# Optimization experiments

Measured on AMD Instinct MI355X. Metric: run time of the kernel, lower is better.

## Reference

```python
import jax, jax.numpy as jnp
import numpy as np

N_NODES = 100000
F_DIM = 128      # graph.num_node_features
TE_DIM = 32      # te_emb_dim
D = F_DIM + TE_DIM  # attention embed_dim = 160
B = 4096         # number of target nodes (batched python loop)
K = 64           # candidates per target
TAU = 1.0
THRESHOLD = 0.2
EPS = 1e-10


def setup_inputs() -> dict:
    key = jax.random.key(0)
    ks = jax.random.split(key, 16)
    inp = {
        "x": jax.random.normal(ks[0], (N_NODES, F_DIM), dtype=jnp.float32),
        "target_node_ids": jax.random.randint(ks[1], (B,), 0, N_NODES),
        "target_node_times": jax.random.randint(ks[2], (B,), 1, 10000),
        "neighbor_ids": jax.random.randint(ks[3], (B, K), 0, N_NODES),
        "edge_time": jax.random.randint(ks[4], (B, K), 0, 10000),
        "edge_weight": jax.random.uniform(ks[5], (B, K), dtype=jnp.float32),
        "gumbel_u": jax.random.uniform(ks[6], (B, K), dtype=jnp.float32),
        # TemporalEncoding params: te(t) = cos(t * w + b)
        "te_w": jax.random.normal(ks[7], (TE_DIM,), dtype=jnp.float32),
        "te_b": jax.random.normal(ks[8], (TE_DIM,), dtype=jnp.float32),
        # MultiheadAttention params (packed qkv like torch)
        "in_proj_w": jax.random.normal(ks[9], (3 * D, D), dtype=jnp.float32) / np.sqrt(D),
        "in_proj_b": jnp.zeros((3 * D,), dtype=jnp.float32),
        "out_w": jax.random.normal(ks[10], (D, D), dtype=jnp.float32) / np.sqrt(D),
        "out_b": jnp.zeros((D,), dtype=jnp.float32),
        # MLP: Linear(D+1 -> 1) + LeakyReLU
        "mlp_w": jax.random.normal(ks[11], (D + 1,), dtype=jnp.float32) / np.sqrt(D + 1),
        "mlp_b": jnp.zeros((1,), dtype=jnp.float32),
    }
    return inp


def reference(x, target_node_ids, target_node_times, neighbor_ids, edge_time,
              edge_weight, gumbel_u, te_w, te_b, in_proj_w, in_proj_b,
              out_w, out_b, mlp_w, mlp_b):
    # --- build target embedding: [B, D]
    t_x = x[target_node_ids]                                          # [B, F]
    t_te = jnp.cos(target_node_times[:, None].astype(jnp.float32) * te_w + te_b)  # [B, TE]
    q_in = jnp.concatenate([t_x, t_te], axis=-1)                      # [B, D]

    # --- candidate embeddings: [B, K, D]
    c_x = x[neighbor_ids]                                             # [B, K, F]
    c_te = jnp.cos(edge_time[..., None].astype(jnp.float32) * te_w + te_b)        # [B, K, TE]
    kv_in = jnp.concatenate([c_x, c_te], axis=-1)                     # [B, K, D]

    # --- single-head MultiheadAttention (eval mode, 1 query per target)
    Wq, Wk, Wv = in_proj_w[:D], in_proj_w[D:2 * D], in_proj_w[2 * D:]
    bq, bk, bv = in_proj_b[:D], in_proj_b[D:2 * D], in_proj_b[2 * D:]
    q = q_in @ Wq.T + bq                                              # [B, D]
    k = jnp.einsum('bkf,df->bkd', kv_in, Wk) + bk                     # [B, K, D]
    v = jnp.einsum('bkf,df->bkd', kv_in, Wv) + bv                     # [B, K, D]
    scores = jnp.einsum('bd,bkd->bk', q, k) / jnp.sqrt(jnp.float32(D))
    attn_w = jax.nn.softmax(scores, axis=-1)                          # [B, K]
    ctx = jnp.einsum('bk,bkd->bd', attn_w, v)                         # [B, D]
    attn_output = ctx @ out_w.T + out_b                               # [B, D]

    # --- gumbel-softmax mask over attention weights (soft, then threshold)
    g = -jnp.log(-jnp.log(gumbel_u + EPS) + EPS)                      # gumbel(0,1)
    y_soft = jax.nn.softmax((attn_w + g) / TAU, axis=-1)
    candidate_mask = y_soft > THRESHOLD                               # [B, K] bool

    # --- MLP edge-weight update: Linear(D+1 -> 1) + LeakyReLU
    mlp_in = jnp.concatenate(
        [jnp.broadcast_to(attn_output[:, None, :], (attn_output.shape[0], edge_weight.shape[1], attn_output.shape[1])),
         edge_weight[..., None]], axis=-1)                            # [B, K, D+1]
    new_edge_weight = jax.nn.leaky_relu(jnp.einsum('bkf,f->bk', mlp_in, mlp_w) + mlp_b[0])  # [B, K]

    return attn_output, new_edge_weight, candidate_mask
```

## Files before the change

### kernel.cpp

```cpp
#include <hip/hip_runtime.h>

#define F_DIM 128
#define TE_DIM 32
#define DD 160
#define NB 4096
#define KK 64
#define ROWS 4
#define LD 164
#define XH_STRIDE 168
#define KT 16

#define WS_M   0
#define WS_V2  25600
#define WS_C   51200
#define WS_U   51360
#define WS_B2  51520
#define WS_S0  51680
#define WS_TE  51684
#define TAB_T  10000
#define TAB_N  (TAB_T * TE_DIM)
#define TAB_BLOCKS 250
#define SETUP_BASE (2 * DD + 3)

__device__ __forceinline__ float dot4acc(const float4 w, const float4 v, float a) {
    a = fmaf(w.x, v.x, a);
    a = fmaf(w.y, v.y, a);
    a = fmaf(w.z, v.z, a);
    a = fmaf(w.w, v.w, a);
    return a;
}

__device__ __forceinline__ float wave_max(float v) {
    #pragma unroll
    for (int off = 32; off > 0; off >>= 1) v = fmaxf(v, __shfl_xor(v, off, 64));
    return v;
}
__device__ __forceinline__ float wave_sum(float v) {
    #pragma unroll
    for (int off = 32; off > 0; off >>= 1) v += __shfl_xor(v, off, 64);
    return v;
}

__device__ __forceinline__ void gemv_rows(
    const float* __restrict__ W, const float* __restrict__ bias,
    const float (*vin)[LD], float (*vout)[LD], int tid)
{
    const int r  = tid & 3;
    const int dl = tid >> 2;
    const float4* v4 = (const float4*)vin[r];
    const float4* w0 = (const float4*)(W + (long)dl * DD);
    const float4* w1 = (const float4*)(W + (long)(dl + 64) * DD);
    float a0 = bias[dl];
    float a1 = bias[dl + 64];
    if (dl < 32) {
        const float4* w2 = (const float4*)(W + (long)(dl + 128) * DD);
        float a2 = bias[dl + 128];
        #pragma unroll 8
        for (int f = 0; f < 40; ++f) {
            const float4 v = v4[f];
            a0 = dot4acc(w0[f], v, a0);
            a1 = dot4acc(w1[f], v, a1);
            a2 = dot4acc(w2[f], v, a2);
        }
        vout[r][dl]       = a0;
        vout[r][dl + 64]  = a1;
        vout[r][dl + 128] = a2;
    } else {
        #pragma unroll 8
        for (int f = 0; f < 40; ++f) {
            const float4 v = v4[f];
            a0 = dot4acc(w0[f], v, a0);
            a1 = dot4acc(w1[f], v, a1);
        }
        vout[r][dl]      = a0;
        vout[r][dl + 64] = a1;
    }
}

__global__ __launch_bounds__(256)
void setup_kernel(const float* __restrict__ ipw, const float* __restrict__ ipb,
                  const float* __restrict__ ow,  const float* __restrict__ ob,
                  const float* __restrict__ te_w, const float* __restrict__ te_b,
                  float* __restrict__ ws)
{
    const int blk = blockIdx.x;
    const int t   = threadIdx.x;
    const float inv = 0.07905694150420949f;

    __shared__ float s_vec[DD];

    if (blk >= SETUP_BASE) {
        const int g0 = (blk - SETUP_BASE) * 256 + t;
        #pragma unroll
        for (int it = 0; it < 5; ++it) {
            const int g = g0 + it * (TAB_BLOCKS * 256);
            const int tt = g >> 5, d = g & 31;
            ws[WS_TE + g] = cosf(fmaf((float)tt, te_w[d], te_b[d]));
        }
        return;
    }

    if (blk < DD) {
        const float* wk = ipw + DD * DD;
        if (t < DD) s_vec[t] = wk[(long)t * DD + blk];
        __syncthreads();
        if (t < DD) {
            float a0 = 0.f, a1 = 0.f, a2 = 0.f, a3 = 0.f;
            #pragma unroll 4
            for (int d = 0; d < DD; d += 4) {
                a0 = fmaf(s_vec[d],     ipw[(long)d * DD + t],       a0);
                a1 = fmaf(s_vec[d + 1], ipw[(long)(d + 1) * DD + t], a1);
                a2 = fmaf(s_vec[d + 2], ipw[(long)(d + 2) * DD + t], a2);
                a3 = fmaf(s_vec[d + 3], ipw[(long)(d + 3) * DD + t], a3);
            }
            ws[WS_M + blk * DD + t] = (a0 + a1 + a2 + a3) * inv;
        }
    } else if (blk < 2 * DD) {
        const int i = blk - DD;
        const float* wv = ipw + 2 * DD * DD;
        if (t < DD) s_vec[t] = ow[(long)i * DD + t];
        __syncthreads();
        if (t < DD) {
            float a0 = 0.f, a1 = 0.f, a2 = 0.f, a3 = 0.f;
            #pragma unroll 4
            for (int d = 0; d < DD; d += 4) {
                a0 = fmaf(s_vec[d],     wv[(long)d * DD + t],       a0);
                a1 = fmaf(s_vec[d + 1], wv[(long)(d + 1) * DD + t], a1);
                a2 = fmaf(s_vec[d + 2], wv[(long)(d + 2) * DD + t], a2);
                a3 = fmaf(s_vec[d + 3], wv[(long)(d + 3) * DD + t], a3);
            }
            ws[WS_V2 + i * DD + t] = a0 + a1 + a2 + a3;
        }
    } else if (blk == 2 * DD) {
        const float* wk = ipw + DD * DD;
        if (t < DD) s_vec[t] = ipb[t];
        __syncthreads();
        if (t < DD) {
            float a0 = 0.f, a1 = 0.f, a2 = 0.f, a3 = 0.f;
            #pragma unroll 4
            for (int d = 0; d < DD; d += 4) {
                a0 = fmaf(s_vec[d],     wk[(long)d * DD + t],       a0);
                a1 = fmaf(s_vec[d + 1], wk[(long)(d + 1) * DD + t], a1);
                a2 = fmaf(s_vec[d + 2], wk[(long)(d + 2) * DD + t], a2);
                a3 = fmaf(s_vec[d + 3], wk[(long)(d + 3) * DD + t], a3);
            }
            ws[WS_C + t] = (a0 + a1 + a2 + a3) * inv;
        }
    } else if (blk == 2 * DD + 1) {
        if (t < DD) s_vec[t] = ipb[DD + t];
        __syncthreads();
        if (t < DD) {
            float a0 = 0.f, a1 = 0.f, a2 = 0.f, a3 = 0.f;
            #pragma unroll 4
            for (int d = 0; d < DD; d += 4) {
                a0 = fmaf(s_vec[d],     ipw[(long)d * DD + t],       a0);
                a1 = fmaf(s_vec[d + 1], ipw[(long)(d + 1) * DD + t], a1);
                a2 = fmaf(s_vec[d + 2], ipw[(long)(d + 2) * DD + t], a2);
                a3 = fmaf(s_vec[d + 3], ipw[(long)(d + 3) * DD + t], a3);
            }
            ws[WS_U + t] = (a0 + a1 + a2 + a3) * inv;
        }
    } else {
        if (t < DD) s_vec[t] = ipb[2 * DD + t];
        __syncthreads();
        if (t < DD) {
            const float* owr = ow + (long)t * DD;
            float a0 = 0.f, a1 = 0.f, a2 = 0.f, a3 = 0.f;
            #pragma unroll 4
            for (int d = 0; d < DD; d += 4) {
                a0 = fmaf(s_vec[d],     owr[d],     a0);
                a1 = fmaf(s_vec[d + 1], owr[d + 1], a1);
                a2 = fmaf(s_vec[d + 2], owr[d + 2], a2);
                a3 = fmaf(s_vec[d + 3], owr[d + 3], a3);
            }
            ws[WS_B2 + t] = ob[t] + (a0 + a1 + a2 + a3);
        }
        if (t >= 192) {
            const int lane = t - 192;
            float p = ipb[lane] * ipb[DD + lane];
            p = fmaf(ipb[lane + 64], ipb[DD + lane + 64], p);
            if (lane < 32) p = fmaf(ipb[lane + 128], ipb[DD + lane + 128], p);
            const float s = wave_sum(p);
            if (lane == 0) ws[WS_S0] = s * inv;
        }
    }
}

__global__ __launch_bounds__(256, 4)
void structure_learner_kernel(
    const float* __restrict__ x,
    const int*   __restrict__ target_node_ids,
    const int*   __restrict__ target_node_times,
    const int*   __restrict__ neighbor_ids,
    const int*   __restrict__ edge_time,
    const float* __restrict__ edge_weight,
    const float* __restrict__ gumbel_u,
    const float* __restrict__ te_w,
    const float* __restrict__ te_b,
    const float* __restrict__ mlp_w,
    const float* __restrict__ mlp_b,
    const float* __restrict__ ws,
    const float* __restrict__ tetab,
    float* __restrict__ out_ao,
    float* __restrict__ out_new,
    float* __restrict__ out_mask)
{
    __shared__ __attribute__((aligned(16))) _Float16 s_xh[ROWS][KT][XH_STRIDE];
    __shared__ __attribute__((aligned(16))) float s_qin[ROWS][LD];
    __shared__ __attribute__((aligned(16))) float s_qt[ROWS][LD];
    __shared__ __attribute__((aligned(16))) float s_wkv[ROWS][LD];
    __shared__ __attribute__((aligned(16))) float s_ao[ROWS][LD];
    __shared__ float s_aw[ROWS][KK];
    __shared__ float s_mt[ROWS][4];
    __shared__ int   s_nid[ROWS][KK];
    __shared__ int   s_et[ROWS][KK];

    const int tid  = threadIdx.x;
    const int wr   = tid >> 6;
    const int lane = tid & 63;
    const int b    = blockIdx.x * ROWS + wr;

    const float* Mw = ws + WS_M;
    const float* V2 = ws + WS_V2;
    const float* Cv = ws + WS_C;
    const float* Uv = ws + WS_U;
    const float* B2 = ws + WS_B2;
    const float  s0 = ws[WS_S0];

    {
        const long eb = (long)b * KK + lane;
        s_nid[wr][lane] = neighbor_ids[eb];
        s_et[wr][lane]  = edge_time[eb];
        const int tn = target_node_ids[b];
        const float2 tx = *(const float2*)(x + (long)tn * F_DIM + lane * 2);
        s_qin[wr][lane * 2]     = tx.x;
        s_qin[wr][lane * 2 + 1] = tx.y;
        if (lane < TE_DIM) {
            const int tt = target_node_times[b];
            s_qin[wr][F_DIM + lane] =
                (tetab && (unsigned)tt < (unsigned)TAB_T)
                    ? tetab[(long)tt * TE_DIM + lane]
                    : cosf(fmaf((float)tt, te_w[lane], te_b[lane]));
        }
    }
    __syncthreads();

    gemv_rows(Mw, Cv, s_qin, s_qt, tid);
    __syncthreads();

    float p = s_qin[wr][lane] * Uv[lane];
    p = fmaf(s_qin[wr][lane + 64], Uv[lane + 64], p);
    if (lane < 32) p = fmaf(s_qin[wr][128 + lane], Uv[128 + lane], p);
    const float sbk = wave_sum(p) + s0;

    const int q = lane >> 2;
    const int j = lane & 3;
    float m_run = -3.0e38f, l_run = 0.f;
    float ax = 0.f, ay = 0.f, at = 0.f;

    for (int t = 0; t < 4; ++t) {
        const int k   = KT * t + q;
        const int nid = s_nid[wr][k];
        const int et  = s_et[wr][k];

        const float4* xr  = (const float4*)(x + (long)nid * F_DIM + 32 * j);
        const float4* qt4 = (const float4*)(s_qt[wr] + 32 * j);
        _Float16* st = &s_xh[wr][q][32 * j];
        float a0 = 0.f, a1 = 0.f;
        #pragma unroll
        for (int f = 0; f < 8; f += 2) {
            const float4 A = xr[f], B = xr[f + 1];
            a0 = dot4acc(A, qt4[f],     a0);
            a1 = dot4acc(B, qt4[f + 1], a1);
            union { _Float16 hh[4]; unsigned long long u; } pa, pb;
            pa.hh[0] = (_Float16)A.x; pa.hh[1] = (_Float16)A.y;
            pa.hh[2] = (_Float16)A.z; pa.hh[3] = (_Float16)A.w;
            pb.hh[0] = (_Float16)B.x; pb.hh[1] = (_Float16)B.y;
            pb.hh[2] = (_Float16)B.z; pb.hh[3] = (_Float16)B.w;
            *(unsigned long long*)&st[4 * f]     = pa.u;
            *(unsigned long long*)&st[4 * f + 4] = pb.u;
        }
        float acc = a0 + a1;

        {
            const float* qte = s_qt[wr] + F_DIM + 8 * j;
            _Float16* stt = &s_xh[wr][q][F_DIM + 8 * j];
            if (tetab && (unsigned)et < (unsigned)TAB_T) {
                const float4* tr = (const float4*)(tetab + (long)et * TE_DIM + 8 * j);
                const float4 T0 = tr[0], T1 = tr[1];
                acc = fmaf(T0.x, qte[0], acc);
                acc = fmaf(T0.y, qte[1], acc);
                acc = fmaf(T0.z, qte[2], acc);
                acc = fmaf(T0.w, qte[3], acc);
                acc = fmaf(T1.x, qte[4], acc);
                acc = fmaf(T1.y, qte[5], acc);
                acc = fmaf(T1.z, qte[6], acc);
                acc = fmaf(T1.w, qte[7], acc);
                union { _Float16 hh[4]; unsigned long long u; } p0, p1;
                p0.hh[0] = (_Float16)T0.x; p0.hh[1] = (_Float16)T0.y;
                p0.hh[2] = (_Float16)T0.z; p0.hh[3] = (_Float16)T0.w;
                p1.hh[0] = (_Float16)T1.x; p1.hh[1] = (_Float16)T1.y;
                p1.hh[2] = (_Float16)T1.z; p1.hh[3] = (_Float16)T1.w;
                *(unsigned long long*)&stt[0] = p0.u;
                *(unsigned long long*)&stt[4] = p1.u;
            } else {
                const float etv = (float)et;
                #pragma unroll
                for (int ii = 0; ii < 8; ++ii) {
                    const float cte = cosf(fmaf(etv, te_w[8 * j + ii], te_b[8 * j + ii]));
                    acc = fmaf(cte, qte[ii], acc);
                    stt[ii] = (_Float16)cte;
                }
            }
        }

        acc += __shfl_xor(acc, 1, 64);
        acc += __shfl_xor(acc, 2, 64);
        const float sc = acc + sbk;

        const float mt   = wave_max(sc);
        const float mnew = fmaxf(m_run, mt);
        const float cfac = expf(m_run - mnew);
        const float e    = expf(sc - mnew);
        l_run = l_run * cfac + wave_sum(e) * 0.25f;
        m_run = mnew;
        if (j == 0)    s_aw[wr][k]  = e;
        if (lane == 0) s_mt[wr][t]  = mnew;
        __syncthreads();

        ax *= cfac; ay *= cfac; at *= cfac;
        #pragma unroll
        for (int qq = 0; qq < KT; ++qq) {
            const float wgt = s_aw[wr][KT * t + qq];
            union { unsigned u; _Float16 h2[2]; } cc;
            cc.u = *(const unsigned*)&s_xh[wr][qq][2 * lane];
            ax = fmaf(wgt, (float)cc.h2[0], ax);
            ay = fmaf(wgt, (float)cc.h2[1], ay);
            if (lane < TE_DIM) at = fmaf(wgt, (float)s_xh[wr][qq][F_DIM + lane], at);
        }
        __syncthreads();
    }

    const float rl = 1.f / l_run;
    s_wkv[wr][lane * 2]     = ax * rl;
    s_wkv[wr][lane * 2 + 1] = ay * rl;
    if (lane < TE_DIM) s_wkv[wr][F_DIM + lane] = at * rl;

    const float u  = gumbel_u[(long)b * KK + lane];
    const float ew = edge_weight[(long)b * KK + lane];
    __syncthreads();

    gemv_rows(V2, B2, s_wkv, s_ao, tid);
    __syncthreads();

    {
        const float awk = s_aw[wr][lane] * expf(s_mt[wr][lane >> 4] - m_run) * rl;

        float pm = s_ao[wr][lane] * mlp_w[lane];
        pm = fmaf(s_ao[wr][lane + 64], mlp_w[lane + 64], pm);
        if (lane < 32) pm = fmaf(s_ao[wr][lane + 128], mlp_w[lane + 128], pm);
        const float base = wave_sum(pm) + mlp_b[0];

        float* ao = out_ao + (long)b * DD;
        ao[lane]      = s_ao[wr][lane];
        ao[lane + 64] = s_ao[wr][lane + 64];
        if (lane < 32) ao[lane + 128] = s_ao[wr][lane + 128];

        const float g = -logf(-logf(u + 1e-10f) + 1e-10f);
        const float z = awk + g;
        const float m = wave_max(z);
        const float e = expf(z - m);
        const float l = wave_sum(e);
        out_mask[(long)b * KK + lane] = (e / l > 0.2f) ? 1.0f : 0.0f;

        const float val = fmaf(ew, mlp_w[DD], base);
        out_new[(long)b * KK + lane] = (val >= 0.f) ? val : 0.01f * val;
    }
}

extern "C" void kernel_launch(void* const* d_in, const int* in_sizes, int n_in,
                              void* d_out, int out_size, void* d_ws, size_t ws_size,
                              hipStream_t stream) {
    const float* x   = (const float*)d_in[0];
    const int*   tni = (const int*)d_in[1];
    const int*   tnt = (const int*)d_in[2];
    const int*   nid = (const int*)d_in[3];
    const int*   et  = (const int*)d_in[4];
    const float* ew  = (const float*)d_in[5];
    const float* gu  = (const float*)d_in[6];
    const float* tew = (const float*)d_in[7];
    const float* teb = (const float*)d_in[8];
    const float* ipw = (const float*)d_in[9];
    const float* ipb = (const float*)d_in[10];
    const float* ow  = (const float*)d_in[11];
    const float* ob  = (const float*)d_in[12];
    const float* mw  = (const float*)d_in[13];
    const float* mb  = (const float*)d_in[14];

    float* wsf = (float*)d_ws;

    float* out      = (float*)d_out;
    float* out_ao   = out;
    float* out_new  = out + (long)NB * DD;
    float* out_mask = out + (long)NB * DD + (long)NB * KK;

    const bool use_tab = ws_size >= (size_t)(WS_TE + TAB_N) * sizeof(float);
    const int  setup_grid = SETUP_BASE + (use_tab ? TAB_BLOCKS : 0);

    setup_kernel<<<setup_grid, 256, 0, stream>>>(ipw, ipb, ow, ob, tew, teb, wsf);

    structure_learner_kernel<<<NB / ROWS, 256, 0, stream>>>(
        x, tni, tnt, nid, et, ew, gu, tew, teb, mw, mb, wsf,
        use_tab ? (wsf + WS_TE) : nullptr,
        out_ao, out_new, out_mask);
}
```

Baseline: 162.4 us.

## Split each target row across two waves with merged online softmax

Each target row is now processed by two wavefronts (512-thread blocks), each handling half of the 64 candidates with its own online softmax, and the partial max and sum are merged through shared memory. The tile per wave shrinks to 8 candidates with 8 lanes per candidate, and the GEMVs are redistributed over 512 threads, with the second GEMV summing the two half-contexts. This is meant to double wave-level parallelism for latency-bound gathers, at the cost of extra shared memory, more block-wide barriers and fewer blocks per CU.

```diff
diff --git a/kernel.cpp b/kernel.cpp
--- a/kernel.cpp
+++ b/kernel.cpp
@@ -8,7 +8,7 @@
 #define ROWS 4
 #define LD 164
 #define XH_STRIDE 168
-#define KT 16
+#define KT 8
 
 #define WS_M   0
 #define WS_V2  25600
@@ -41,7 +41,7 @@
     return v;
 }
 
-__device__ __forceinline__ void gemv_rows(
+__device__ __forceinline__ void gemv512(
     const float* __restrict__ W, const float* __restrict__ bias,
     const float (*vin)[LD], float (*vout)[LD], int tid)
 {
@@ -49,31 +49,58 @@
     const int dl = tid >> 2;
     const float4* v4 = (const float4*)vin[r];
     const float4* w0 = (const float4*)(W + (long)dl * DD);
-    const float4* w1 = (const float4*)(W + (long)(dl + 64) * DD);
     float a0 = bias[dl];
-    float a1 = bias[dl + 64];
     if (dl < 32) {
-        const float4* w2 = (const float4*)(W + (long)(dl + 128) * DD);
-        float a2 = bias[dl + 128];
+        const float4* w1 = (const float4*)(W + (long)(dl + 128) * DD);
+        float a1 = bias[dl + 128];
         #pragma unroll 8
         for (int f = 0; f < 40; ++f) {
             const float4 v = v4[f];
             a0 = dot4acc(w0[f], v, a0);
             a1 = dot4acc(w1[f], v, a1);
-            a2 = dot4acc(w2[f], v, a2);
         }
         vout[r][dl]       = a0;
-        vout[r][dl + 64]  = a1;
-        vout[r][dl + 128] = a2;
+        vout[r][dl + 128] = a1;
     } else {
         #pragma unroll 8
         for (int f = 0; f < 40; ++f) {
             const float4 v = v4[f];
             a0 = dot4acc(w0[f], v, a0);
+        }
+        vout[r][dl] = a0;
+    }
+}
+
+__device__ __forceinline__ void gemv512_2(
+    const float* __restrict__ W, const float* __restrict__ bias,
+    const float (*vin)[2][LD], float (*vout)[LD], int tid)
+{
+    const int r  = tid & 3;
+    const int dl = tid >> 2;
+    const float4* va = (const float4*)vin[r][0];
+    const float4* vb = (const float4*)vin[r][1];
+    const float4* w0 = (const float4*)(W + (long)dl * DD);
+    float a0 = bias[dl];
+    if (dl < 32) {
+        const float4* w1 = (const float4*)(W + (long)(dl + 128) * DD);
+        float a1 = bias[dl + 128];
+        #pragma unroll 8
+        for (int f = 0; f < 40; ++f) {
+            const float4 A = va[f], B = vb[f];
+            float4 v; v.x = A.x + B.x; v.y = A.y + B.y; v.z = A.z + B.z; v.w = A.w + B.w;
+            a0 = dot4acc(w0[f], v, a0);
             a1 = dot4acc(w1[f], v, a1);
         }
-        vout[r][dl]      = a0;
-        vout[r][dl + 64] = a1;
+        vout[r][dl]       = a0;
+        vout[r][dl + 128] = a1;
+    } else {
+        #pragma unroll 8
+        for (int f = 0; f < 40; ++f) {
+            const float4 A = va[f], B = vb[f];
+            float4 v; v.x = A.x + B.x; v.y = A.y + B.y; v.z = A.z + B.z; v.w = A.w + B.w;
+            a0 = dot4acc(w0[f], v, a0);
+        }
+        vout[r][dl] = a0;
     }
 }
 
@@ -186,7 +213,7 @@
     }
 }
 
-__global__ __launch_bounds__(256, 4)
+__global__ __launch_bounds__(512, 4)
 void structure_learner_kernel(
     const float* __restrict__ x,
     const int*   __restrict__ target_node_ids,
@@ -205,19 +232,22 @@
     float* __restrict__ out_new,
     float* __restrict__ out_mask)
 {
-    __shared__ __attribute__((aligned(16))) _Float16 s_xh[ROWS][KT][XH_STRIDE];
+    __shared__ __attribute__((aligned(16))) _Float16 s_xh[ROWS][2][KT][XH_STRIDE];
     __shared__ __attribute__((aligned(16))) float s_qin[ROWS][LD];
     __shared__ __attribute__((aligned(16))) float s_qt[ROWS][LD];
-    __shared__ __attribute__((aligned(16))) float s_wkv[ROWS][LD];
+    __shared__ __attribute__((aligned(16))) float s_wkvh[ROWS][2][LD];
     __shared__ __attribute__((aligned(16))) float s_ao[ROWS][LD];
-    __shared__ float s_aw[ROWS][KK];
-    __shared__ float s_mt[ROWS][4];
-    __shared__ int   s_nid[ROWS][KK];
-    __shared__ int   s_et[ROWS][KK];
+    __shared__ float  s_aw[ROWS][KK];
+    __shared__ float  s_mt[ROWS][2][4];
+    __shared__ float2 s_ml[ROWS][2];
+    __shared__ int    s_nid[ROWS][KK];
+    __shared__ int    s_et[ROWS][KK];
 
     const int tid  = threadIdx.x;
-    const int wr   = tid >> 6;
+    const int w    = tid >> 6;
     const int lane = tid & 63;
+    const int wr   = w >> 1;
+    const int h    = w & 1;
     const int b    = blockIdx.x * ROWS + wr;
 
     const float* Mw = ws + WS_M;
@@ -229,23 +259,26 @@
 
     {
         const long eb = (long)b * KK + lane;
-        s_nid[wr][lane] = neighbor_ids[eb];
-        s_et[wr][lane]  = edge_time[eb];
-        const int tn = target_node_ids[b];
-        const float2 tx = *(const float2*)(x + (long)tn * F_DIM + lane * 2);
-        s_qin[wr][lane * 2]     = tx.x;
-        s_qin[wr][lane * 2 + 1] = tx.y;
-        if (lane < TE_DIM) {
-            const int tt = target_node_times[b];
-            s_qin[wr][F_DIM + lane] =
-                (tetab && (unsigned)tt < (unsigned)TAB_T)
-                    ? tetab[(long)tt * TE_DIM + lane]
-                    : cosf(fmaf((float)tt, te_w[lane], te_b[lane]));
+        if (h == 0) {
+            s_nid[wr][lane] = neighbor_ids[eb];
+            const int tn = target_node_ids[b];
+            const float2 tx = *(const float2*)(x + (long)tn * F_DIM + lane * 2);
+            s_qin[wr][lane * 2]     = tx.x;
+            s_qin[wr][lane * 2 + 1] = tx.y;
+        } else {
+            s_et[wr][lane] = edge_time[eb];
+            if (lane < TE_DIM) {
+                const int tt = target_node_times[b];
+                s_qin[wr][F_DIM + lane] =
+                    (tetab && (unsigned)tt < (unsigned)TAB_T)
+                        ? tetab[(long)tt * TE_DIM + lane]
+                        : cosf(fmaf((float)tt, te_w[lane], te_b[lane]));
+            }
         }
     }
     __syncthreads();
 
-    gemv_rows(Mw, Cv, s_qin, s_qt, tid);
+    gemv512(Mw, Cv, s_qin, s_qt, tid);
     __syncthreads();
 
     float p = s_qin[wr][lane] * Uv[lane];
@@ -253,22 +286,22 @@
     if (lane < 32) p = fmaf(s_qin[wr][128 + lane], Uv[128 + lane], p);
     const float sbk = wave_sum(p) + s0;
 
-    const int q = lane >> 2;
-    const int j = lane & 3;
+    const int q = lane >> 3;
+    const int j = lane & 7;
     float m_run = -3.0e38f, l_run = 0.f;
     float ax = 0.f, ay = 0.f, at = 0.f;
 
-    for (int t = 0; t < 4; ++t) {
-        const int k   = KT * t + q;
+    for (int ti = 0; ti < 4; ++ti) {
+        const int k   = 32 * h + KT * ti + q;
         const int nid = s_nid[wr][k];
         const int et  = s_et[wr][k];
 
-        const float4* xr  = (const float4*)(x + (long)nid * F_DIM + 32 * j);
-        const float4* qt4 = (const float4*)(s_qt[wr] + 32 * j);
-        _Float16* st = &s_xh[wr][q][32 * j];
+        const float4* xr  = (const float4*)(x + (long)nid * F_DIM + 16 * j);
+        const float4* qt4 = (const float4*)(s_qt[wr] + 16 * j);
+        _Float16* st = &s_xh[wr][h][q][16 * j];
         float a0 = 0.f, a1 = 0.f;
         #pragma unroll
-        for (int f = 0; f < 8; f += 2) {
+        for (int f = 0; f < 4; f += 2) {
             const float4 A = xr[f], B = xr[f + 1];
             a0 = dot4acc(A, qt4[f],     a0);
             a1 = dot4acc(B, qt4[f + 1], a1);
@@ -283,31 +316,23 @@
         float acc = a0 + a1;
 
         {
-            const float* qte = s_qt[wr] + F_DIM + 8 * j;
-            _Float16* stt = &s_xh[wr][q][F_DIM + 8 * j];
+            const float* qte = s_qt[wr] + F_DIM + 4 * j;
+            _Float16* stt = &s_xh[wr][h][q][F_DIM + 4 * j];
             if (tetab && (unsigned)et < (unsigned)TAB_T) {
-                const float4* tr = (const float4*)(tetab + (long)et * TE_DIM + 8 * j);
-                const float4 T0 = tr[0], T1 = tr[1];
-                acc = fmaf(T0.x, qte[0], acc);
-                acc = fmaf(T0.y, qte[1], acc);
-                acc = fmaf(T0.z, qte[2], acc);
-                acc = fmaf(T0.w, qte[3], acc);
-                acc = fmaf(T1.x, qte[4], acc);
-                acc = fmaf(T1.y, qte[5], acc);
-                acc = fmaf(T1.z, qte[6], acc);
-                acc = fmaf(T1.w, qte[7], acc);
-                union { _Float16 hh[4]; unsigned long long u; } p0, p1;
-                p0.hh[0] = (_Float16)T0.x; p0.hh[1] = (_Float16)T0.y;
-                p0.hh[2] = (_Float16)T0.z; p0.hh[3] = (_Float16)T0.w;
-                p1.hh[0] = (_Float16)T1.x; p1.hh[1] = (_Float16)T1.y;
-                p1.hh[2] = (_Float16)T1.z; p1.hh[3] = (_Float16)T1.w;
-                *(unsigned long long*)&stt[0] = p0.u;
-                *(unsigned long long*)&stt[4] = p1.u;
+                const float4 T = *(const float4*)(tetab + (long)et * TE_DIM + 4 * j);
+                acc = fmaf(T.x, qte[0], acc);
+                acc = fmaf(T.y, qte[1], acc);
+                acc = fmaf(T.z, qte[2], acc);
+                acc = fmaf(T.w, qte[3], acc);
+                union { _Float16 hh[4]; unsigned long long u; } pt;
+                pt.hh[0] = (_Float16)T.x; pt.hh[1] = (_Float16)T.y;
+                pt.hh[2] = (_Float16)T.z; pt.hh[3] = (_Float16)T.w;
+                *(unsigned long long*)&stt[0] = pt.u;
             } else {
                 const float etv = (float)et;
                 #pragma unroll
-                for (int ii = 0; ii < 8; ++ii) {
-                    const float cte = cosf(fmaf(etv, te_w[8 * j + ii], te_b[8 * j + ii]));
+                for (int ii = 0; ii < 4; ++ii) {
+                    const float cte = cosf(fmaf(etv, te_w[4 * j + ii], te_b[4 * j + ii]));
                     acc = fmaf(cte, qte[ii], acc);
                     stt[ii] = (_Float16)cte;
                 }
@@ -316,45 +341,57 @@
 
         acc += __shfl_xor(acc, 1, 64);
         acc += __shfl_xor(acc, 2, 64);
+        acc += __shfl_xor(acc, 4, 64);
         const float sc = acc + sbk;
 
         const float mt   = wave_max(sc);
         const float mnew = fmaxf(m_run, mt);
         const float cfac = expf(m_run - mnew);
         const float e    = expf(sc - mnew);
-        l_run = l_run * cfac + wave_sum(e) * 0.25f;
+        l_run = l_run * cfac + wave_sum(e) * 0.125f;
         m_run = mnew;
-        if (j == 0)    s_aw[wr][k]  = e;
-        if (lane == 0) s_mt[wr][t]  = mnew;
+        if (j == 0)    s_aw[wr][k]      = e;
+        if (lane == 0) s_mt[wr][h][ti]  = mnew;
         __syncthreads();
 
         ax *= cfac; ay *= cfac; at *= cfac;
         #pragma unroll
         for (int qq = 0; qq < KT; ++qq) {
-            const float wgt = s_aw[wr][KT * t + qq];
+            const float wgt = s_aw[wr][32 * h + KT * ti + qq];
             union { unsigned u; _Float16 h2[2]; } cc;
-            cc.u = *(const unsigned*)&s_xh[wr][qq][2 * lane];
+            cc.u = *(const unsigned*)&s_xh[wr][h][qq][2 * lane];
             ax = fmaf(wgt, (float)cc.h2[0], ax);
             ay = fmaf(wgt, (float)cc.h2[1], ay);
-            if (lane < TE_DIM) at = fmaf(wgt, (float)s_xh[wr][qq][F_DIM + lane], at);
-        }
-        __syncthreads();
-    }
-
-    const float rl = 1.f / l_run;
-    s_wkv[wr][lane * 2]     = ax * rl;
-    s_wkv[wr][lane * 2 + 1] = ay * rl;
-    if (lane < TE_DIM) s_wkv[wr][F_DIM + lane] = at * rl;
-
-    const float u  = gumbel_u[(long)b * KK + lane];
-    const float ew = edge_weight[(long)b * KK + lane];
+            if (lane < TE_DIM) at = fmaf(wgt, (float)s_xh[wr][h][qq][F_DIM + lane], at);
+        }
+        __syncthreads();
+    }
+
+    if (lane == 0) s_ml[wr][h] = make_float2(m_run, l_run);
     __syncthreads();
-
-    gemv_rows(V2, B2, s_wkv, s_ao, tid);
+    const float2 M0 = s_ml[wr][0], M1 = s_ml[wr][1];
+    const float  mF = fmaxf(M0.x, M1.x);
+    const float  lF = M0.y * expf(M0.x - mF) + M1.y * expf(M1.x - mF);
+    const float  sch = expf(m_run - mF) / lF;
+
+    s_wkvh[wr][h][lane * 2]     = ax * sch;
+    s_wkvh[wr][h][lane * 2 + 1] = ay * sch;
+    if (lane < TE_DIM) s_wkvh[wr][h][F_DIM + lane] = at * sch;
+
+    float u = 0.f, ew = 0.f;
+    if (h == 0) {
+        u  = gumbel_u[(long)b * KK + lane];
+        ew = edge_weight[(long)b * KK + lane];
+    }
     __syncthreads();
 
-    {
-        const float awk = s_aw[wr][lane] * expf(s_mt[wr][lane >> 4] - m_run) * rl;
+    gemv512_2(V2, B2, s_wkvh, s_ao, tid);
+    __syncthreads();
+
+    if (h == 0) {
+        const int   hk = lane >> 5;
+        const int   tk = (lane & 31) >> 3;
+        const float aw = s_aw[wr][lane] * expf(s_mt[wr][hk][tk] - mF) / lF;
 
         float pm = s_ao[wr][lane] * mlp_w[lane];
         pm = fmaf(s_ao[wr][lane + 64], mlp_w[lane + 64], pm);
@@ -367,7 +404,7 @@
         if (lane < 32) ao[lane + 128] = s_ao[wr][lane + 128];
 
         const float g = -logf(-logf(u + 1e-10f) + 1e-10f);
-        const float z = awk + g;
+        const float z = aw + g;
         const float m = wave_max(z);
         const float e = expf(z - m);
         const float l = wave_sum(e);
@@ -409,7 +446,7 @@
 
     setup_kernel<<<setup_grid, 256, 0, stream>>>(ipw, ipb, ow, ob, tew, teb, wsf);
 
-    structure_learner_kernel<<<NB / ROWS, 256, 0, stream>>>(
+    structure_learner_kernel<<<NB / ROWS, 512, 0, stream>>>(
         x, tni, tnt, nid, et, ew, gu, tew, teb, mw, mb, wsf,
         use_tab ? (wsf + WS_TE) : nullptr,
         out_ao, out_new, out_mask);
```

After: 167.7 us. 3.2% more time.
